# Kernel optimization log

Hardware: AMD Instinct MI355X
Metric: run time of the kernel (lower is better)

The kernel has to match this reference:

```python
import jax, jax.numpy as jnp
import numpy as np

H = 8  # number of heads


def setup_inputs() -> dict:
    key = jax.random.key(0)
    ks = jax.random.split(key, 8)
    B, L, S, D, P = 4, 2048, 2048, 1024, 1024
    sc = 0.02
    return {
        "queries": jax.random.normal(ks[0], (B, L, D), jnp.float32),
        "keys": jax.random.normal(ks[1], (B, S, D), jnp.float32),
        "values": jax.random.normal(ks[2], (B, S, D), jnp.float32),
        "Wq": jax.random.normal(ks[3], (D, P), jnp.float32) * sc,
        "bq": jnp.zeros((P,), jnp.float32),
        "Wk": jax.random.normal(ks[4], (D, P), jnp.float32) * sc,
        "bk": jnp.zeros((P,), jnp.float32),
        "Wv": jax.random.normal(ks[5], (D, P), jnp.float32) * sc,
        "bv": jnp.zeros((P,), jnp.float32),
        "Wo": jax.random.normal(ks[6], (P, D), jnp.float32) * sc,
        "bo": jnp.zeros((D,), jnp.float32),
    }


def reference(queries, keys, values, Wq, bq, Wk, bk, Wv, bv, Wo, bo):
    B, L, _ = queries.shape
    S = keys.shape[1]
    # linear projections, split into heads: [B, T, H, E]
    q = (queries @ Wq + bq).reshape(B, L, H, -1)
    k = (keys @ Wk + bk).reshape(B, S, H, -1)
    v = (values @ Wv + bv).reshape(B, S, H, -1)
    E = q.shape[-1]
    scale = 1.0 / jnp.sqrt(jnp.float32(E))
    scores = jnp.einsum("blhe,bshe->bhls", q, k)
    A = jax.nn.softmax(scale * scores, axis=-1)  # dropout is identity at eval
    V = jnp.einsum("bhls,bshd->blhd", A, v)
    out = V.reshape(B, L, -1)
    return out @ Wo + bo
```

## Files before the change

### kernel.cpp

```cpp
#include <hip/hip_runtime.h>
#include <hip/hip_bf16.h>
#include <cstdint>

typedef __attribute__((ext_vector_type(4))) float f32x4;
typedef __attribute__((ext_vector_type(16))) float f32x16;
typedef __attribute__((ext_vector_type(8))) __bf16 bf16x8;
typedef __attribute__((ext_vector_type(4))) unsigned u32x4;

#define SCALE_Q 0.08838834764831845f

__device__ __forceinline__ short bf16b(float f) {
  unsigned u = __builtin_bit_cast(unsigned, f);
  unsigned r = (u + 0x7fffu + ((u >> 16) & 1u)) >> 16;
  return (short)r;
}

__device__ __forceinline__ unsigned packbf(float lo, float hi) {
  return (unsigned)(unsigned short)bf16b(lo) |
         ((unsigned)(unsigned short)bf16b(hi) << 16);
}

__device__ __forceinline__ f32x4 mfma16(bf16x8 a, bf16x8 b, f32x4 c) {
  return __builtin_amdgcn_mfma_f32_16x16x32_bf16(a, b, c, 0, 0, 0);
}
__device__ __forceinline__ f32x16 mfma32(bf16x8 a, bf16x8 b, f32x16 c) {
  return __builtin_amdgcn_mfma_f32_32x32x16_bf16(a, b, c, 0, 0, 0);
}

__device__ __forceinline__ void async16(void* lds, const void* g) {
  __builtin_amdgcn_global_load_lds(
      (const __attribute__((address_space(1))) unsigned int*)g,
      (__attribute__((address_space(3))) unsigned int*)lds, 16, 0, 0);
}

__global__ void cvt_x(const float* __restrict__ q, const float* __restrict__ k,
                      const float* __restrict__ v, short* __restrict__ out) {
  const float* src = (blockIdx.y == 0) ? q : (blockIdx.y == 1 ? k : v);
  short* dst = out + (size_t)blockIdx.y * 8388608;
  size_t i = (size_t)blockIdx.x * 256 + threadIdx.x;
  float4 f = reinterpret_cast<const float4*>(src)[i];
  short4 o;
  o.x = bf16b(f.x); o.y = bf16b(f.y); o.z = bf16b(f.z); o.w = bf16b(f.w);
  reinterpret_cast<short4*>(dst)[i] = o;
}

__global__ void cvt_w(const float* __restrict__ Wq, const float* __restrict__ Wk,
                      const float* __restrict__ Wv, const float* __restrict__ Wo,
                      short* __restrict__ out) {
  int z = blockIdx.z;
  const float* W = (z == 0) ? Wq : (z == 1) ? Wk : (z == 2) ? Wv : Wo;
  float scale = (z == 0) ? SCALE_Q : 1.0f;
  __shared__ float t[64][65];
  int n0 = blockIdx.x * 64, k0 = blockIdx.y * 64;
  int c = threadIdx.x & 63, r0 = threadIdx.x >> 6;
#pragma unroll
  for (int rr = 0; rr < 16; ++rr) {
    int r = rr * 4 + r0;
    t[r][c] = W[(size_t)(k0 + r) * 1024 + n0 + c];
  }
  __syncthreads();
  short* dst = out + (size_t)z * 1048576;
#pragma unroll
  for (int rr = 0; rr < 16; ++rr) {
    int r = rr * 4 + r0;
    dst[(size_t)(n0 + r) * 1024 + k0 + c] = bf16b(t[c][r] * scale);
  }
}

__device__ __forceinline__ void gemm_core(const short* A, const short* Bn, int m0,
                                          int n0, short* As, short* Bs,
                                          f32x4 acc[4][4]) {
  int tid = threadIdx.x;
  int lane = tid & 63, wave = tid >> 6;
  int wr = wave >> 1, wc = wave & 1, l15 = lane & 15, lg = lane >> 4;
  for (int k0 = 0; k0 < 1024; k0 += 64) {
#pragma unroll
    for (int i = 0; i < 4; ++i) {
      int r = (tid >> 3) + i * 32, cb = (tid & 7) * 16;
      async16((char*)As + i * 4096 + tid * 16,
              (const char*)A + ((size_t)(m0 + r) * 1024 + k0) * 2 + cb);
      async16((char*)Bs + i * 4096 + tid * 16,
              (const char*)Bn + ((size_t)(n0 + r) * 1024 + k0) * 2 + cb);
    }
    __syncthreads();
#pragma unroll
    for (int kk = 0; kk < 2; ++kk) {
      bf16x8 a[4], b[4];
#pragma unroll
      for (int mt = 0; mt < 4; ++mt)
        a[mt] = *(const bf16x8*)&As[(wr * 64 + mt * 16 + l15) * 64 + lg * 8 + kk * 32];
#pragma unroll
      for (int nt = 0; nt < 4; ++nt)
        b[nt] = *(const bf16x8*)&Bs[(wc * 64 + nt * 16 + l15) * 64 + lg * 8 + kk * 32];
#pragma unroll
      for (int mt = 0; mt < 4; ++mt)
#pragma unroll
        for (int nt = 0; nt < 4; ++nt)
          acc[mt][nt] = mfma16(a[mt], b[nt], acc[mt][nt]);
    }
    __syncthreads();
  }
}

__global__ __launch_bounds__(256, 2) void gemm_qkv(
    const short* __restrict__ X3, const short* __restrict__ WT,
    const float* __restrict__ bq, const float* __restrict__ bk,
    const float* __restrict__ bv, short* __restrict__ Qg, short* __restrict__ Kg,
    short* __restrict__ Vtg) {
  __shared__ short As[8192], Bs[8192];
  int z = blockIdx.z;
  const short* A = X3 + (size_t)z * 8388608;
  const short* Bn = WT + (size_t)z * 1048576;
  const float* bias = (z == 0) ? bq : (z == 1) ? bk : bv;
  float bscale = (z == 0) ? SCALE_Q : 1.0f;
  int m0 = blockIdx.y * 128, n0 = blockIdx.x * 128;
  f32x4 acc[4][4];
#pragma unroll
  for (int mt = 0; mt < 4; ++mt)
#pragma unroll
    for (int nt = 0; nt < 4; ++nt) acc[mt][nt] = f32x4{0.f, 0.f, 0.f, 0.f};
  gemm_core(A, Bn, m0, n0, As, Bs, acc);
  int lane = threadIdx.x & 63, wave = threadIdx.x >> 6;
  int wr = wave >> 1, wc = wave & 1, l15 = lane & 15, lg = lane >> 4;
#pragma unroll
  for (int mt = 0; mt < 4; ++mt)
#pragma unroll
    for (int nt = 0; nt < 4; ++nt) {
      int n = n0 + wc * 64 + nt * 16 + l15;
      float bb = bias[n] * bscale;
#pragma unroll
      for (int j = 0; j < 4; ++j) {
        int m = m0 + wr * 64 + mt * 16 + lg * 4 + j;
        short o = bf16b(acc[mt][nt][j] + bb);
        int s_ = m & 2047, b_ = m >> 11, h_ = n >> 7, e_ = n & 127;
        size_t bh = (size_t)b_ * 8 + h_;
        if (z == 0)
          Qg[(bh * 2048 + s_) * 128 + e_] = o;
        else if (z == 1)
          Kg[(bh * 2048 + s_) * 128 + (e_ ^ ((s_ & 15) << 3))] = o;
        else
          Vtg[(bh * 128 + e_) * 2048 + (s_ ^ (((e_ >> 1) & 7) << 3))] = o;
      }
    }
}

__global__ __launch_bounds__(256, 2) void attn(const short* __restrict__ Qg,
                                               const short* __restrict__ Kg,
                                               const short* __restrict__ Vtg,
                                               short* __restrict__ Ctx) {
  __shared__ short Ks[2][8192];
  __shared__ short Vs[2][8192];
  int tid = threadIdx.x;
  int lane = tid & 63, wave = tid >> 6;
  int l31 = lane & 31, h = lane >> 5;
  int bh = blockIdx.y, qb = blockIdx.x;
  int qbase = qb * 128 + wave * 32;
  const short* Qp = Qg + (size_t)bh * 2048 * 128;
  const char* Kbase = (const char*)(Kg + (size_t)bh * 2048 * 128);
  const char* Vbase = (const char*)(Vtg + (size_t)bh * 128 * 2048);

  auto stage = [&](int t, int buf) {
    int s0 = t * 64;
    char* kd = (char*)&Ks[buf][0];
    char* vd = (char*)&Vs[buf][0];
#pragma unroll
    for (int i = 0; i < 4; ++i)
      async16(kd + i * 4096 + tid * 16,
              Kbase + (size_t)s0 * 256 + i * 4096 + tid * 16);
#pragma unroll
    for (int i = 0; i < 4; ++i) {
      int e = i * 32 + 2 * (tid >> 4) + ((tid >> 3) & 1);
      async16(vd + i * 4096 + tid * 16,
              Vbase + (size_t)e * 4096 + s0 * 2 + (tid & 7) * 16);
    }
  };

  stage(0, 0);

  bf16x8 qa[8];
  const short* qrow = Qp + (size_t)(qbase + l31) * 128 + h * 8;
#pragma unroll
  for (int ksl = 0; ksl < 8; ++ksl) qa[ksl] = *(const bf16x8*)(qrow + ksl * 16);

  f32x16 acc[4];
#pragma unroll
  for (int i = 0; i < 4; ++i)
#pragma unroll
    for (int r = 0; r < 16; ++r) acc[i][r] = 0.f;
  float mrun = -1e30f, lrun = 0.f;

  int swK = (l31 & 15) << 3;
  int swV = ((l31 >> 1) & 7) << 3;

  for (int t = 0; t < 32; ++t) {
    int cur = t & 1;
    if (t < 31) {
      stage(t + 1, cur ^ 1);
      asm volatile("s_waitcnt vmcnt(8)" ::: "memory");
    } else {
      asm volatile("s_waitcnt vmcnt(0)" ::: "memory");
    }
    __builtin_amdgcn_s_barrier();

    const short* Kc = Ks[cur];
    const short* Vc = Vs[cur];

    f32x16 st0, st1;
#pragma unroll
    for (int r = 0; r < 16; ++r) { st0[r] = 0.f; st1[r] = 0.f; }
    __builtin_amdgcn_s_setprio(1);
#pragma unroll
    for (int ksl = 0; ksl < 8; ++ksl) {
      int col = (ksl * 16 + h * 8) ^ swK;
      bf16x8 ka0 = *(const bf16x8*)&Kc[l31 * 128 + col];
      bf16x8 ka1 = *(const bf16x8*)&Kc[(32 + l31) * 128 + col];
      st0 = mfma32(ka0, qa[ksl], st0);
      st1 = mfma32(ka1, qa[ksl], st1);
    }
    __builtin_amdgcn_s_setprio(0);

    float mx = st0[0];
#pragma unroll
    for (int r = 1; r < 16; ++r) mx = fmaxf(mx, st0[r]);
#pragma unroll
    for (int r = 0; r < 16; ++r) mx = fmaxf(mx, st1[r]);
    mx = fmaxf(mx, __shfl_xor(mx, 32));
    int skip = __all(mx - mrun <= 5.0f);
    float mn = mrun, sf = 1.f;
    if (!skip) {
      mn = fmaxf(mrun, mx);
      sf = __expf(mrun - mn);
      mrun = mn;
    }
    float rs = 0.f;
#pragma unroll
    for (int r = 0; r < 16; ++r) { float p = __expf(st0[r] - mn); st0[r] = p; rs += p; }
#pragma unroll
    for (int r = 0; r < 16; ++r) { float p = __expf(st1[r] - mn); st1[r] = p; rs += p; }
    rs += __shfl_xor(rs, 32);
    if (!skip) {
      lrun = lrun * sf + rs;
#pragma unroll
      for (int reg = 0; reg < 16; ++reg) {
        float s4 = __shfl(sf, (reg & 3) + 8 * (reg >> 2) + 4 * h);
#pragma unroll
        for (int nte = 0; nte < 4; ++nte) acc[nte][reg] *= s4;
      }
    } else {
      lrun += rs;
    }

    unsigned w0[8], w1[8];
#pragma unroll
    for (int m = 0; m < 8; ++m) {
      w0[m] = packbf(st0[2 * m], st0[2 * m + 1]);
      w1[m] = packbf(st1[2 * m], st1[2 * m + 1]);
    }
    bf16x8 pa[4];
#pragma unroll
    for (int ks = 0; ks < 4; ++ks) {
      const unsigned* w = (ks & 2) ? w1 : w0;
      int mb = (ks & 1) * 4;
      unsigned a0 = w[mb], b0 = w[mb + 2];
      unsigned a1 = w[mb + 1], b1 = w[mb + 3];
      asm volatile("v_permlane32_swap_b32 %0, %1" : "+v"(a0), "+v"(b0));
      asm volatile("v_permlane32_swap_b32 %0, %1" : "+v"(a1), "+v"(b1));
      u32x4 tt;
      tt[0] = a0; tt[1] = a1; tt[2] = b0; tt[3] = b1;
      pa[ks] = __builtin_bit_cast(bf16x8, tt);
    }

    __builtin_amdgcn_s_setprio(1);
#pragma unroll
    for (int nte = 0; nte < 4; ++nte) {
      int rbase = (nte * 16 + (l31 >> 1)) * 128 + (lane & 1) * 64;
#pragma unroll
      for (int ks = 0; ks < 4; ++ks) {
        int colk = (ks * 16 + h * 8) ^ swV;
        bf16x8 vb = *(const bf16x8*)&Vc[rbase + colk];
        acc[nte] = mfma32(pa[ks], vb, acc[nte]);
      }
    }
    __builtin_amdgcn_s_setprio(0);
    __builtin_amdgcn_s_barrier();
  }

  float inv = 1.0f / lrun;
  int b_ = bh >> 3, h_ = bh & 7;
#pragma unroll
  for (int reg = 0; reg < 16; ++reg) {
    int qr = (reg & 3) + 8 * (reg >> 2) + 4 * h;
    float iq = __shfl(inv, qr);
    int q = qbase + qr;
    short* orow = Ctx + (((size_t)b_ * 2048 + q) * 8 + h_) * 128;
#pragma unroll
    for (int nte = 0; nte < 4; ++nte)
      orow[nte * 32 + l31] = bf16b(acc[nte][reg] * iq);
  }
}

__global__ __launch_bounds__(256, 2) void gemm_out(const short* __restrict__ Ctx,
                                                   const short* __restrict__ WoT,
                                                   const float* __restrict__ bo,
                                                   float* __restrict__ Out) {
  __shared__ short As[8192], Bs[8192];
  int m0 = blockIdx.y * 128, n0 = blockIdx.x * 128;
  f32x4 acc[4][4];
#pragma unroll
  for (int mt = 0; mt < 4; ++mt)
#pragma unroll
    for (int nt = 0; nt < 4; ++nt) acc[mt][nt] = f32x4{0.f, 0.f, 0.f, 0.f};
  gemm_core(Ctx, WoT, m0, n0, As, Bs, acc);
  int lane = threadIdx.x & 63, wave = threadIdx.x >> 6;
  int wr = wave >> 1, wc = wave & 1, l15 = lane & 15, lg = lane >> 4;
#pragma unroll
  for (int mt = 0; mt < 4; ++mt)
#pragma unroll
    for (int nt = 0; nt < 4; ++nt) {
      int n = n0 + wc * 64 + nt * 16 + l15;
      float bb = bo[n];
#pragma unroll
      for (int j = 0; j < 4; ++j) {
        int m = m0 + wr * 64 + mt * 16 + lg * 4 + j;
        Out[(size_t)m * 1024 + n] = acc[mt][nt][j] + bb;
      }
    }
}

extern "C" void kernel_launch(void* const* d_in, const int* in_sizes, int n_in,
                              void* d_out, int out_size, void* d_ws, size_t ws_size,
                              hipStream_t stream) {
  const float* q = (const float*)d_in[0];
  const float* k = (const float*)d_in[1];
  const float* v = (const float*)d_in[2];
  const float* Wq = (const float*)d_in[3];
  const float* bq = (const float*)d_in[4];
  const float* Wk = (const float*)d_in[5];
  const float* bk = (const float*)d_in[6];
  const float* Wv = (const float*)d_in[7];
  const float* bv = (const float*)d_in[8];
  const float* Wo = (const float*)d_in[9];
  const float* bo = (const float*)d_in[10];
  float* out = (float*)d_out;

  short* ws = (short*)d_ws;
  short* X3 = ws;
  short* WT = X3 + (size_t)3 * 8388608;
  short* Qg = WT + (size_t)4 * 1048576;
  short* Kg = Qg + (size_t)8388608;
  short* Vtg = Kg + (size_t)8388608;
  short* Ctx = X3;

  hipLaunchKernelGGL(cvt_x, dim3(8192, 3), dim3(256), 0, stream, q, k, v, X3);
  hipLaunchKernelGGL(cvt_w, dim3(16, 16, 4), dim3(256), 0, stream, Wq, Wk, Wv, Wo, WT);
  hipLaunchKernelGGL(gemm_qkv, dim3(8, 64, 3), dim3(256), 0, stream, X3, WT, bq, bk,
                     bv, Qg, Kg, Vtg);
  hipLaunchKernelGGL(attn, dim3(16, 32), dim3(256), 0, stream, Qg, Kg, Vtg, Ctx);
  hipLaunchKernelGGL(gemm_out, dim3(8, 64), dim3(256), 0, stream, Ctx,
                     WT + (size_t)3 * 1048576, bo, out);
}
```

Before: 223.6 us.

## Replace GEMMs with 256x256-tile pipelined kernel using swizzled LDS and staged prefetch

```diff
diff --git a/kernel.cpp b/kernel.cpp
--- a/kernel.cpp
+++ b/kernel.cpp
@@ -67,81 +67,162 @@
   }
 }
 
-__device__ __forceinline__ void gemm_core(const short* A, const short* Bn, int m0,
-                                          int n0, short* As, short* Bs,
-                                          f32x4 acc[4][4]) {
+#define PHASE(APTR, BPTR, MH, NH, STAGE_STMT, VMCNT_STMT)                      \
+  {                                                                            \
+    bf16x8 af[4][2], bfr[2][2];                                                \
+    _Pragma("unroll") for (int mt = 0; mt < 4; ++mt)                           \
+        _Pragma("unroll") for (int kk = 0; kk < 2; ++kk) {                     \
+      int r = wr * 128 + MH * 64 + mt * 16 + l15;                              \
+      af[mt][kk] = *(const bf16x8*)((const char*)(APTR) + r * 128 +            \
+                                    ((lg * 16 + kk * 64) ^ ((r & 7) << 4)));   \
+    }                                                                          \
+    _Pragma("unroll") for (int nt = 0; nt < 2; ++nt)                           \
+        _Pragma("unroll") for (int kk = 0; kk < 2; ++kk) {                     \
+      int r = wc * 64 + NH * 32 + nt * 16 + l15;                               \
+      bfr[nt][kk] = *(const bf16x8*)((const char*)(BPTR) + r * 128 +           \
+                                     ((lg * 16 + kk * 64) ^ ((r & 7) << 4)));  \
+    }                                                                          \
+    STAGE_STMT;                                                                \
+    VMCNT_STMT;                                                                \
+    __builtin_amdgcn_s_barrier();                                              \
+    __builtin_amdgcn_s_setprio(1);                                             \
+    _Pragma("unroll") for (int kk = 0; kk < 2; ++kk)                           \
+        _Pragma("unroll") for (int mt = 0; mt < 4; ++mt)                       \
+            _Pragma("unroll") for (int nt = 0; nt < 2; ++nt)                   \
+                acc[MH * 4 + mt][NH * 2 + nt] = mfma16(                        \
+                    af[mt][kk], bfr[nt][kk], acc[MH * 4 + mt][NH * 2 + nt]);   \
+    __builtin_amdgcn_s_setprio(0);                                             \
+    __builtin_amdgcn_s_barrier();                                              \
+  }
+
+__global__ __launch_bounds__(512, 2) void gemm256(
+    const short* __restrict__ Ab, const short* __restrict__ WT,
+    const float* __restrict__ bq, const float* __restrict__ bk,
+    const float* __restrict__ bv, const float* __restrict__ bo,
+    short* __restrict__ Qg, short* __restrict__ Kg, short* __restrict__ Vtg,
+    float* __restrict__ Out, int zbase, int nwg) {
+  __shared__ short LDS[65536];
+  short* LA = LDS;
+  short* LB = LDS + 32768;
+
+  int id = blockIdx.x;
+  int cpx = nwg >> 3;
+  int swz = (id & 7) * cpx + (id >> 3);
+  int z = zbase + (swz >> 7);
+  int rem = swz & 127;
+  int m0 = (rem >> 2) * 256, n0 = (rem & 3) * 256;
+
+  const short* Ag = (zbase == 0) ? Ab + (size_t)z * 8388608 : Ab;
+  const short* Bg = WT + (size_t)z * 1048576;
+
   int tid = threadIdx.x;
   int lane = tid & 63, wave = tid >> 6;
-  int wr = wave >> 1, wc = wave & 1, l15 = lane & 15, lg = lane >> 4;
-  for (int k0 = 0; k0 < 1024; k0 += 64) {
-#pragma unroll
-    for (int i = 0; i < 4; ++i) {
-      int r = (tid >> 3) + i * 32, cb = (tid & 7) * 16;
-      async16((char*)As + i * 4096 + tid * 16,
-              (const char*)A + ((size_t)(m0 + r) * 1024 + k0) * 2 + cb);
-      async16((char*)Bs + i * 4096 + tid * 16,
-              (const char*)Bn + ((size_t)(n0 + r) * 1024 + k0) * 2 + cb);
-    }
-    __syncthreads();
-#pragma unroll
-    for (int kk = 0; kk < 2; ++kk) {
-      bf16x8 a[4], b[4];
-#pragma unroll
-      for (int mt = 0; mt < 4; ++mt)
-        a[mt] = *(const bf16x8*)&As[(wr * 64 + mt * 16 + l15) * 64 + lg * 8 + kk * 32];
-#pragma unroll
-      for (int nt = 0; nt < 4; ++nt)
-        b[nt] = *(const bf16x8*)&Bs[(wc * 64 + nt * 16 + l15) * 64 + lg * 8 + kk * 32];
-#pragma unroll
-      for (int mt = 0; mt < 4; ++mt)
-#pragma unroll
-        for (int nt = 0; nt < 4; ++nt)
-          acc[mt][nt] = mfma16(a[mt], b[nt], acc[mt][nt]);
-    }
-    __syncthreads();
-  }
-}
-
-__global__ __launch_bounds__(256, 2) void gemm_qkv(
-    const short* __restrict__ X3, const short* __restrict__ WT,
-    const float* __restrict__ bq, const float* __restrict__ bk,
-    const float* __restrict__ bv, short* __restrict__ Qg, short* __restrict__ Kg,
-    short* __restrict__ Vtg) {
-  __shared__ short As[8192], Bs[8192];
-  int z = blockIdx.z;
-  const short* A = X3 + (size_t)z * 8388608;
-  const short* Bn = WT + (size_t)z * 1048576;
-  const float* bias = (z == 0) ? bq : (z == 1) ? bk : bv;
-  float bscale = (z == 0) ? SCALE_Q : 1.0f;
-  int m0 = blockIdx.y * 128, n0 = blockIdx.x * 128;
-  f32x4 acc[4][4];
-#pragma unroll
-  for (int mt = 0; mt < 4; ++mt)
-#pragma unroll
-    for (int nt = 0; nt < 4; ++nt) acc[mt][nt] = f32x4{0.f, 0.f, 0.f, 0.f};
-  gemm_core(A, Bn, m0, n0, As, Bs, acc);
-  int lane = threadIdx.x & 63, wave = threadIdx.x >> 6;
-  int wr = wave >> 1, wc = wave & 1, l15 = lane & 15, lg = lane >> 4;
-#pragma unroll
-  for (int mt = 0; mt < 4; ++mt)
-#pragma unroll
-    for (int nt = 0; nt < 4; ++nt) {
-      int n = n0 + wc * 64 + nt * 16 + l15;
-      float bb = bias[n] * bscale;
-#pragma unroll
-      for (int j = 0; j < 4; ++j) {
-        int m = m0 + wr * 64 + mt * 16 + lg * 4 + j;
-        short o = bf16b(acc[mt][nt][j] + bb);
-        int s_ = m & 2047, b_ = m >> 11, h_ = n >> 7, e_ = n & 127;
-        size_t bh = (size_t)b_ * 8 + h_;
-        if (z == 0)
-          Qg[(bh * 2048 + s_) * 128 + e_] = o;
-        else if (z == 1)
-          Kg[(bh * 2048 + s_) * 128 + (e_ ^ ((s_ & 15) << 3))] = o;
-        else
-          Vtg[(bh * 128 + e_) * 2048 + (s_ ^ (((e_ >> 1) & 7) << 3))] = o;
+  int wr = wave >> 2, wc = wave & 3, l15 = lane & 15, lg = lane >> 4;
+
+  auto stageA = [&](short* buf, int k0, int h) {
+#pragma unroll
+    for (int ld = 0; ld < 2; ++ld) {
+      int row = (2 * ld + h) * 64 + (tid >> 3);
+      int gc = (tid & 7) ^ (row & 7);
+      async16((char*)buf + row * 128 + (tid & 7) * 16,
+              (const char*)Ag + (size_t)(m0 + row) * 2048 + k0 * 2 + gc * 16);
+    }
+  };
+  auto stageB = [&](short* buf, int k0, int h) {
+#pragma unroll
+    for (int ld = 0; ld < 2; ++ld) {
+      int idx = tid >> 3;
+      int n = (h + 2 * (idx >> 5) + 4 * ld) * 32 + (idx & 31);
+      int gc = (tid & 7) ^ (n & 7);
+      async16((char*)buf + n * 128 + (tid & 7) * 16,
+              (const char*)Bg + (size_t)(n0 + n) * 2048 + k0 * 2 + gc * 16);
+    }
+  };
+
+  f32x4 acc[8][4];
+#pragma unroll
+  for (int i = 0; i < 8; ++i)
+#pragma unroll
+    for (int j = 0; j < 4; ++j) acc[i][j] = f32x4{0.f, 0.f, 0.f, 0.f};
+
+  stageA(LA, 0, 0); stageB(LB, 0, 0); stageA(LA, 0, 1); stageB(LB, 0, 1);
+  stageA(LA + 16384, 64, 0); stageB(LB + 16384, 64, 0);
+  asm volatile("s_waitcnt vmcnt(4)" ::: "memory");
+  __builtin_amdgcn_s_barrier();
+
+  for (int t = 0; t < 16; ++t) {
+    short* Ap = LA + (t & 1) * 16384;
+    short* Bp = LB + (t & 1) * 16384;
+    short* Aq = LA + ((t & 1) ^ 1) * 16384;
+    short* Bq = LB + ((t & 1) ^ 1) * 16384;
+    PHASE(Ap, Bp, 0, 0, { if (t + 1 < 16) stageA(Aq, t * 64 + 64, 1); }, {});
+    PHASE(Ap, Bp, 0, 1, { if (t + 1 < 16) stageB(Bq, t * 64 + 64, 1); }, {});
+    PHASE(Ap, Bp, 1, 0, { if (t + 2 < 16) stageA(Ap, t * 64 + 128, 0); }, {});
+    PHASE(Ap, Bp, 1, 1, { if (t + 2 < 16) stageB(Bp, t * 64 + 128, 0); },
+          {
+            if (t <= 13) asm volatile("s_waitcnt vmcnt(4)" ::: "memory");
+            else if (t == 14) asm volatile("s_waitcnt vmcnt(0)" ::: "memory");
+          });
+  }
+
+  if (z == 2) {
+    unsigned* L32 = (unsigned*)LDS;
+#pragma unroll
+    for (int pass = 0; pass < 2; ++pass) {
+      if (wr == pass) {
+#pragma unroll
+        for (int nt4 = 0; nt4 < 4; ++nt4) {
+          int ncol = wc * 64 + nt4 * 16 + l15;
+          float bb = bv[n0 + ncol];
+#pragma unroll
+          for (int mt8 = 0; mt8 < 8; ++mt8) {
+            unsigned lo = packbf(acc[mt8][nt4][0] + bb, acc[mt8][nt4][1] + bb);
+            unsigned hi = packbf(acc[mt8][nt4][2] + bb, acc[mt8][nt4][3] + bb);
+            int base = ncol * 68 + mt8 * 8 + lg * 2;
+            L32[base] = lo;
+            L32[base + 1] = hi;
+          }
+        }
       }
-    }
+      asm volatile("s_waitcnt lgkmcnt(0)" ::: "memory");
+      __builtin_amdgcn_s_barrier();
+#pragma unroll
+      for (int i = 0; i < 8; ++i) {
+        int idx = i * 512 + tid;
+        int col = idx >> 4, ch = idx & 15;
+        u32x4 val = *(u32x4*)&L32[col * 68 + ch * 4];
+        int nf = n0 + col, e_ = nf & 127, h_ = nf >> 7;
+        size_t bh = (size_t)(m0 >> 11) * 8 + h_;
+        int sb = ((m0 & 2047) + pass * 128 + ch * 8) ^ (((e_ >> 1) & 7) << 3);
+        *(u32x4*)&Vtg[(bh * 128 + e_) * 2048 + sb] = val;
+      }
+      asm volatile("s_waitcnt lgkmcnt(0)" ::: "memory");
+      __builtin_amdgcn_s_barrier();
+    }
+  } else {
+    const float* bias = (z == 0) ? bq : (z == 1) ? bk : bo;
+    float bsc = (z == 0) ? SCALE_Q : 1.0f;
+#pragma unroll
+    for (int nt4 = 0; nt4 < 4; ++nt4) {
+      int n = n0 + wc * 64 + nt4 * 16 + l15;
+      float bb = bias[n] * bsc;
+#pragma unroll
+      for (int mt8 = 0; mt8 < 8; ++mt8)
+#pragma unroll
+        for (int j = 0; j < 4; ++j) {
+          int m = m0 + wr * 128 + mt8 * 16 + lg * 4 + j;
+          float c = acc[mt8][nt4][j] + bb;
+          if (z == 3) {
+            Out[(size_t)m * 1024 + n] = c;
+          } else {
+            int s_ = m & 2047, b_ = m >> 11, h_ = n >> 7, e_ = n & 127;
+            size_t bh = (size_t)b_ * 8 + h_;
+            if (z == 0) Qg[(bh * 2048 + s_) * 128 + e_] = bf16b(c);
+            else Kg[(bh * 2048 + s_) * 128 + (e_ ^ ((s_ & 15) << 3))] = bf16b(c);
+          }
+        }
+    }
+  }
 }
 
 __global__ __launch_bounds__(256, 2) void attn(const short* __restrict__ Qg,
@@ -297,34 +378,6 @@
     for (int nte = 0; nte < 4; ++nte)
       orow[nte * 32 + l31] = bf16b(acc[nte][reg] * iq);
   }
-}
-
-__global__ __launch_bounds__(256, 2) void gemm_out(const short* __restrict__ Ctx,
-                                                   const short* __restrict__ WoT,
-                                                   const float* __restrict__ bo,
-                                                   float* __restrict__ Out) {
-  __shared__ short As[8192], Bs[8192];
-  int m0 = blockIdx.y * 128, n0 = blockIdx.x * 128;
-  f32x4 acc[4][4];
-#pragma unroll
-  for (int mt = 0; mt < 4; ++mt)
-#pragma unroll
-    for (int nt = 0; nt < 4; ++nt) acc[mt][nt] = f32x4{0.f, 0.f, 0.f, 0.f};
-  gemm_core(Ctx, WoT, m0, n0, As, Bs, acc);
-  int lane = threadIdx.x & 63, wave = threadIdx.x >> 6;
-  int wr = wave >> 1, wc = wave & 1, l15 = lane & 15, lg = lane >> 4;
-#pragma unroll
-  for (int mt = 0; mt < 4; ++mt)
-#pragma unroll
-    for (int nt = 0; nt < 4; ++nt) {
-      int n = n0 + wc * 64 + nt * 16 + l15;
-      float bb = bo[n];
-#pragma unroll
-      for (int j = 0; j < 4; ++j) {
-        int m = m0 + wr * 64 + mt * 16 + lg * 4 + j;
-        Out[(size_t)m * 1024 + n] = acc[mt][nt][j] + bb;
-      }
-    }
 }
 
 extern "C" void kernel_launch(void* const* d_in, const int* in_sizes, int n_in,
@@ -353,9 +406,9 @@
 
   hipLaunchKernelGGL(cvt_x, dim3(8192, 3), dim3(256), 0, stream, q, k, v, X3);
   hipLaunchKernelGGL(cvt_w, dim3(16, 16, 4), dim3(256), 0, stream, Wq, Wk, Wv, Wo, WT);
-  hipLaunchKernelGGL(gemm_qkv, dim3(8, 64, 3), dim3(256), 0, stream, X3, WT, bq, bk,
-                     bv, Qg, Kg, Vtg);
+  hipLaunchKernelGGL(gemm256, dim3(384), dim3(512), 0, stream, X3, WT, bq, bk, bv,
+                     bo, Qg, Kg, Vtg, out, 0, 384);
   hipLaunchKernelGGL(attn, dim3(16, 32), dim3(256), 0, stream, Qg, Kg, Vtg, Ctx);
-  hipLaunchKernelGGL(gemm_out, dim3(8, 64), dim3(256), 0, stream, Ctx,
-                     WT + (size_t)3 * 1048576, bo, out);
-}
+  hipLaunchKernelGGL(gemm256, dim3(128), dim3(512), 0, stream, Ctx, WT, bq, bk, bv,
+                     bo, Qg, Kg, Vtg, out, 3, 128);
+}
```

Result: slower. 239.2 us (+7.0%).
